# Kernel optimization log

Hardware: AMD Instinct MI355X
Metric: run time of the kernel (lower is better)

Reference implementation:

```python
import jax, jax.numpy as jnp
import numpy as np

NUM_LAYERS = 2
IN_DIM = 256
OUT_DIM = 256
N = 8192


def setup_inputs() -> dict:
    key = jax.random.key(0)
    k = jax.random.split(key, 7)
    x = jax.random.normal(k[0], (N, IN_DIM), dtype=jnp.float32)
    adj = jax.random.uniform(k[1], (N, N), dtype=jnp.float32)
    # MLP params (Linear: y = x @ W.T + b); kaiming-ish scale
    W1 = jax.random.normal(k[2], (OUT_DIM, IN_DIM), dtype=jnp.float32) / np.sqrt(IN_DIM)
    b1 = jnp.zeros((OUT_DIM,), dtype=jnp.float32)
    W2 = jax.random.normal(k[3], (OUT_DIM, OUT_DIM), dtype=jnp.float32) / np.sqrt(OUT_DIM)
    b2 = jnp.zeros((OUT_DIM,), dtype=jnp.float32)
    epsilon = jnp.zeros((1,), dtype=jnp.float32)  # torch init: Tensor([0.0])
    return {"x": x, "adj": adj, "W1": W1, "b1": b1, "W2": W2, "b2": b2, "epsilon": epsilon}


def reference(x, adj, W1, b1, W2, b2, epsilon):
    for _ in range(NUM_LAYERS):
        # epsilon-weighted neighborhood aggregation + residual
        x = x + epsilon * (adj @ x)          # [N, d]
        # 2-layer MLP (shared across layers, as in the torch module)
        h = jax.nn.relu(x @ W1.T + b1)       # [N, out]
        x = h @ W2.T + b2                    # [N, out]
    return x
```

## Files before the change

kernel.cpp:

```cpp
#include <hip/hip_runtime.h>
#include <hip/hip_bf16.h>

typedef __hip_bfloat16 bf16;
typedef short s16x8 __attribute__((ext_vector_type(8)));
typedef float f32x4 __attribute__((ext_vector_type(4)));

static constexpr int NROWS = 8192;
static constexpr int DIM   = 256;

__device__ inline float to_f(float v) { return v; }
__device__ inline float to_f(bf16 v)  { return __bfloat162float(v); }
__device__ inline unsigned short f2bf(float f) {
    bf16 h = __float2bfloat16(f);
    return __builtin_bit_cast(unsigned short, h);
}

__global__ void agg0_convW_kernel(const float* __restrict__ x, const float* __restrict__ adj,
                                  const float* __restrict__ W1, const float* __restrict__ W2,
                                  const float* __restrict__ eps_p,
                                  bf16* __restrict__ W1b, bf16* __restrict__ W2b,
                                  float* __restrict__ y) {
    {
        const int b = blockIdx.x;
        const float* src = (b < 64) ? W1 : W2;
        bf16*       dst = (b < 64) ? W1b : W2b;
        const int t = (b & 63) * 256 + threadIdx.x;
        float4 v = ((const float4*)src)[t];
        ushort4 u = make_ushort4(f2bf(v.x), f2bf(v.y), f2bf(v.z), f2bf(v.w));
        ((ushort4*)dst)[t] = u;
    }
    const float eps = *eps_p;
    if (eps == 0.0f) return;
    const size_t total = (size_t)NROWS * DIM;
    for (size_t e = (size_t)blockIdx.x * blockDim.x + threadIdx.x;
         e < total;
         e += (size_t)gridDim.x * blockDim.x) {
        const int i = (int)(e >> 8);
        const int j = (int)(e & 255);
        float s = 0.0f;
        const float* arow = adj + (size_t)i * NROWS;
        for (int k = 0; k < NROWS; ++k)
            s += arow[k] * x[(size_t)k * DIM + j];
        y[e] = x[e] + eps * s;
    }
}

__global__ void agg1_kernel(const bf16* __restrict__ x, const float* __restrict__ adj,
                            const float* __restrict__ eps_p, bf16* __restrict__ y) {
    const float eps = *eps_p;
    if (eps == 0.0f) return;
    const size_t total = (size_t)NROWS * DIM;
    for (size_t e = (size_t)blockIdx.x * blockDim.x + threadIdx.x;
         e < total;
         e += (size_t)gridDim.x * blockDim.x) {
        const int i = (int)(e >> 8);
        const int j = (int)(e & 255);
        float s = 0.0f;
        const float* arow = adj + (size_t)i * NROWS;
        for (int k = 0; k < NROWS; ++k)
            s += arow[k] * to_f(x[(size_t)k * DIM + j]);
        y[e] = __float2bfloat16(to_f(x[e]) + eps * s);
    }
}

template<typename TIN, bool RELU, bool OUTF32>
__global__ __launch_bounds__(256, 2)
void gemm_bt(const TIN* __restrict__ A0, const TIN* __restrict__ A1,
             const float* __restrict__ eps_p,
             const bf16* __restrict__ W, const float* __restrict__ bias,
             void* __restrict__ C) {
    constexpr int K = 256;
    constexpr int PITCH = 264;
    __shared__ short As[64][PITCH];
    __shared__ short Bs[64][PITCH];

    const TIN* __restrict__ A = (*eps_p == 0.0f) ? A0 : A1;

    const int tid  = threadIdx.x;
    const int lane = tid & 63;
    const int wave = tid >> 6;
    const int wm = (wave & 1) * 32;
    const int wn = (wave >> 1) * 32;
    const int row0 = blockIdx.x * 64;
    const int col0 = blockIdx.y * 64;

#pragma unroll
    for (int p = 0; p < 8; ++p) {
        const int id = p * 256 + tid;
        const int r  = id >> 5;
        const int c  = (id & 31) * 8;
        if constexpr (sizeof(TIN) == 4) {
            const float* src = (const float*)A + (size_t)(row0 + r) * K + c;
            float4 v0 = *(const float4*)(src);
            float4 v1 = *(const float4*)(src + 4);
            ushort4 u0 = make_ushort4(f2bf(v0.x), f2bf(v0.y), f2bf(v0.z), f2bf(v0.w));
            ushort4 u1 = make_ushort4(f2bf(v1.x), f2bf(v1.y), f2bf(v1.z), f2bf(v1.w));
            *(ushort4*)(&As[r][c])     = u0;
            *(ushort4*)(&As[r][c + 4]) = u1;
        } else {
            *(uint4*)(&As[r][c]) = *(const uint4*)((const bf16*)A + (size_t)(row0 + r) * K + c);
        }
        *(uint4*)(&Bs[r][c]) = *(const uint4*)(W + (size_t)(col0 + r) * K + c);
    }
    __syncthreads();

    const int lr = lane & 15;
    const int q  = lane >> 4;
    f32x4 acc[2][2] = {};
#pragma unroll
    for (int kk = 0; kk < 8; ++kk) {
        s16x8 af[2], bf_[2];
#pragma unroll
        for (int i = 0; i < 2; ++i) {
            af[i]  = *(const s16x8*)(&As[wm + i * 16 + lr][kk * 32 + q * 8]);
            bf_[i] = *(const s16x8*)(&Bs[wn + i * 16 + lr][kk * 32 + q * 8]);
        }
#pragma unroll
        for (int i = 0; i < 2; ++i)
#pragma unroll
            for (int j = 0; j < 2; ++j)
                acc[i][j] = __builtin_amdgcn_mfma_f32_16x16x32_bf16(
                    af[i], bf_[j], acc[i][j], 0, 0, 0);
    }

#pragma unroll
    for (int i = 0; i < 2; ++i) {
#pragma unroll
        for (int j = 0; j < 2; ++j) {
            const int col = col0 + wn + j * 16 + lr;
            const float bv = bias[col];
#pragma unroll
            for (int r = 0; r < 4; ++r) {
                const int row = row0 + wm + i * 16 + q * 4 + r;
                float v = acc[i][j][r] + bv;
                if (RELU) v = fmaxf(v, 0.0f);
                if (OUTF32) ((float*)C)[(size_t)row * DIM + col] = v;
                else        ((bf16*)C)[(size_t)row * DIM + col] = __float2bfloat16(v);
            }
        }
    }
}

extern "C" void kernel_launch(void* const* d_in, const int* in_sizes, int n_in,
                              void* d_out, int out_size, void* d_ws, size_t ws_size,
                              hipStream_t stream) {
    const float* x   = (const float*)d_in[0];
    const float* adj = (const float*)d_in[1];
    const float* W1  = (const float*)d_in[2];
    const float* b1  = (const float*)d_in[3];
    const float* W2  = (const float*)d_in[4];
    const float* b2  = (const float*)d_in[5];
    const float* eps = (const float*)d_in[6];
    float* out = (float*)d_out;

    char* ws = (char*)d_ws;
    bf16*  W1b   = (bf16*)ws;  ws += (size_t)DIM * DIM * 2;
    bf16*  W2b   = (bf16*)ws;  ws += (size_t)DIM * DIM * 2;
    bf16*  bufY0 = (bf16*)ws;  ws += (size_t)NROWS * DIM * 2;
    bf16*  bufY1 = (bf16*)ws;  ws += (size_t)NROWS * DIM * 2;
    bf16*  bufY2 = (bf16*)ws;  ws += (size_t)NROWS * DIM * 2;
    float* agg0  = (float*)ws; ws += (size_t)NROWS * DIM * 4;
    bf16*  agg1  = (bf16*)ws;  ws += (size_t)NROWS * DIM * 2;

    const dim3 ggrid(NROWS / 64, DIM / 64);

    agg0_convW_kernel<<<128, 256, 0, stream>>>(x, adj, W1, W2, eps, W1b, W2b, agg0);
    gemm_bt<float, true,  false><<<ggrid, 256, 0, stream>>>(x,     agg0, eps, W1b, b1, bufY0);
    gemm_bt<bf16,  false, false><<<ggrid, 256, 0, stream>>>(bufY0, bufY0, eps, W2b, b2, bufY1);

    agg1_kernel<<<128, 256, 0, stream>>>(bufY1, adj, eps, agg1);
    gemm_bt<bf16,  true,  false><<<ggrid, 256, 0, stream>>>(bufY1, agg1, eps, W1b, b1, bufY2);
    gemm_bt<bf16,  false, true ><<<ggrid, 256, 0, stream>>>(bufY2, bufY2, eps, W2b, b2, out);
}
```

Baseline: 327.6 us.

## Fuse both MLP linears and aggregation into one kernel per layer

Replaces the separate aggregation kernels and four GEMM launches with one fused kernel per layer that optionally aggregates, computes the first linear with ReLU into shared memory, then the second linear. The hidden activation stays in LDS instead of round-tripping through global memory, and launch count drops. Weight fragments are now read directly from global/L2 rather than staged in LDS, and the fallback aggregation path for nonzero epsilon is a naive per-row loop.

Measured after the change: 331.9 us. Within noise of the previous version (+1.3%).

```diff
diff --git a/kernel.cpp b/kernel.cpp
--- a/kernel.cpp
+++ b/kernel.cpp
@@ -15,125 +15,128 @@
     return __builtin_bit_cast(unsigned short, h);
 }
 
-__global__ void agg0_convW_kernel(const float* __restrict__ x, const float* __restrict__ adj,
-                                  const float* __restrict__ W1, const float* __restrict__ W2,
-                                  const float* __restrict__ eps_p,
-                                  bf16* __restrict__ W1b, bf16* __restrict__ W2b,
-                                  float* __restrict__ y) {
-    {
-        const int b = blockIdx.x;
-        const float* src = (b < 64) ? W1 : W2;
-        bf16*       dst = (b < 64) ? W1b : W2b;
-        const int t = (b & 63) * 256 + threadIdx.x;
-        float4 v = ((const float4*)src)[t];
-        ushort4 u = make_ushort4(f2bf(v.x), f2bf(v.y), f2bf(v.z), f2bf(v.w));
-        ((ushort4*)dst)[t] = u;
-    }
-    const float eps = *eps_p;
-    if (eps == 0.0f) return;
-    const size_t total = (size_t)NROWS * DIM;
-    for (size_t e = (size_t)blockIdx.x * blockDim.x + threadIdx.x;
-         e < total;
-         e += (size_t)gridDim.x * blockDim.x) {
-        const int i = (int)(e >> 8);
-        const int j = (int)(e & 255);
-        float s = 0.0f;
-        const float* arow = adj + (size_t)i * NROWS;
-        for (int k = 0; k < NROWS; ++k)
-            s += arow[k] * x[(size_t)k * DIM + j];
-        y[e] = x[e] + eps * s;
-    }
+__global__ void convW_kernel(const float* __restrict__ W1, const float* __restrict__ W2,
+                             bf16* __restrict__ W1b, bf16* __restrict__ W2b) {
+    const int b = blockIdx.x;
+    const float* src = (b < 64) ? W1 : W2;
+    bf16*       dst = (b < 64) ? W1b : W2b;
+    const int t = (b & 63) * 256 + threadIdx.x;
+    float4 v = ((const float4*)src)[t];
+    ((ushort4*)dst)[t] = make_ushort4(f2bf(v.x), f2bf(v.y), f2bf(v.z), f2bf(v.w));
 }
 
-__global__ void agg1_kernel(const bf16* __restrict__ x, const float* __restrict__ adj,
-                            const float* __restrict__ eps_p, bf16* __restrict__ y) {
-    const float eps = *eps_p;
-    if (eps == 0.0f) return;
-    const size_t total = (size_t)NROWS * DIM;
-    for (size_t e = (size_t)blockIdx.x * blockDim.x + threadIdx.x;
-         e < total;
-         e += (size_t)gridDim.x * blockDim.x) {
-        const int i = (int)(e >> 8);
-        const int j = (int)(e & 255);
-        float s = 0.0f;
-        const float* arow = adj + (size_t)i * NROWS;
-        for (int k = 0; k < NROWS; ++k)
-            s += arow[k] * to_f(x[(size_t)k * DIM + j]);
-        y[e] = __float2bfloat16(to_f(x[e]) + eps * s);
-    }
-}
-
-template<typename TIN, bool RELU, bool OUTF32>
-__global__ __launch_bounds__(256, 2)
-void gemm_bt(const TIN* __restrict__ A0, const TIN* __restrict__ A1,
-             const float* __restrict__ eps_p,
-             const bf16* __restrict__ W, const float* __restrict__ bias,
-             void* __restrict__ C) {
+template<typename TIN, bool OUTF32>
+__global__ __launch_bounds__(256, 1)
+void fused_mlp(const TIN* __restrict__ A, const float* __restrict__ adj,
+               const float* __restrict__ eps_p,
+               const bf16* __restrict__ W1, const float* __restrict__ b1,
+               const bf16* __restrict__ W2, const float* __restrict__ b2,
+               void* __restrict__ C) {
     constexpr int K = 256;
     constexpr int PITCH = 264;
-    __shared__ short As[64][PITCH];
-    __shared__ short Bs[64][PITCH];
-
-    const TIN* __restrict__ A = (*eps_p == 0.0f) ? A0 : A1;
+    __shared__ short Xs[32][PITCH];
+    __shared__ short Hs[32][PITCH];
 
     const int tid  = threadIdx.x;
     const int lane = tid & 63;
     const int wave = tid >> 6;
-    const int wm = (wave & 1) * 32;
-    const int wn = (wave >> 1) * 32;
-    const int row0 = blockIdx.x * 64;
-    const int col0 = blockIdx.y * 64;
+    const int lr = lane & 15;
+    const int q  = lane >> 4;
+    const int row0 = blockIdx.x * 32;
+    const float eps = *eps_p;
 
+    if (eps == 0.0f) {
 #pragma unroll
-    for (int p = 0; p < 8; ++p) {
-        const int id = p * 256 + tid;
-        const int r  = id >> 5;
-        const int c  = (id & 31) * 8;
-        if constexpr (sizeof(TIN) == 4) {
-            const float* src = (const float*)A + (size_t)(row0 + r) * K + c;
-            float4 v0 = *(const float4*)(src);
-            float4 v1 = *(const float4*)(src + 4);
-            ushort4 u0 = make_ushort4(f2bf(v0.x), f2bf(v0.y), f2bf(v0.z), f2bf(v0.w));
-            ushort4 u1 = make_ushort4(f2bf(v1.x), f2bf(v1.y), f2bf(v1.z), f2bf(v1.w));
-            *(ushort4*)(&As[r][c])     = u0;
-            *(ushort4*)(&As[r][c + 4]) = u1;
-        } else {
-            *(uint4*)(&As[r][c]) = *(const uint4*)((const bf16*)A + (size_t)(row0 + r) * K + c);
+        for (int p = 0; p < 4; ++p) {
+            const int id = p * 256 + tid;
+            const int r  = id >> 5;
+            const int c  = (id & 31) * 8;
+            if constexpr (sizeof(TIN) == 4) {
+                const float* src = (const float*)A + (size_t)(row0 + r) * K + c;
+                float4 v0 = *(const float4*)(src);
+                float4 v1 = *(const float4*)(src + 4);
+                *(ushort4*)(&Xs[r][c])     = make_ushort4(f2bf(v0.x), f2bf(v0.y), f2bf(v0.z), f2bf(v0.w));
+                *(ushort4*)(&Xs[r][c + 4]) = make_ushort4(f2bf(v1.x), f2bf(v1.y), f2bf(v1.z), f2bf(v1.w));
+            } else {
+                *(uint4*)(&Xs[r][c]) = *(const uint4*)((const bf16*)A + (size_t)(row0 + r) * K + c);
+            }
         }
-        *(uint4*)(&Bs[r][c]) = *(const uint4*)(W + (size_t)(col0 + r) * K + c);
+    } else {
+        for (int r = 0; r < 32; ++r) {
+            const int row = row0 + r;
+            float s = 0.0f;
+            const float* arow = adj + (size_t)row * NROWS;
+            for (int k = 0; k < NROWS; ++k)
+                s += arow[k] * to_f(A[(size_t)k * DIM + tid]);
+            Xs[r][tid] = (short)f2bf(to_f(A[(size_t)row * DIM + tid]) + eps * s);
+        }
     }
     __syncthreads();
 
-    const int lr = lane & 15;
-    const int q  = lane >> 4;
-    f32x4 acc[2][2] = {};
+    f32x4 acc1[4][2] = {};
+    const bf16* W1p = W1 + (size_t)(wave * 64 + lr) * K + q * 8;
 #pragma unroll
     for (int kk = 0; kk < 8; ++kk) {
-        s16x8 af[2], bf_[2];
+        s16x8 wf[4], xf[2];
 #pragma unroll
-        for (int i = 0; i < 2; ++i) {
-            af[i]  = *(const s16x8*)(&As[wm + i * 16 + lr][kk * 32 + q * 8]);
-            bf_[i] = *(const s16x8*)(&Bs[wn + i * 16 + lr][kk * 32 + q * 8]);
+        for (int i = 0; i < 4; ++i)
+            wf[i] = *(const s16x8*)(W1p + (size_t)i * 16 * K + kk * 32);
+#pragma unroll
+        for (int j = 0; j < 2; ++j)
+            xf[j] = *(const s16x8*)(&Xs[j * 16 + lr][kk * 32 + q * 8]);
+#pragma unroll
+        for (int i = 0; i < 4; ++i)
+#pragma unroll
+            for (int j = 0; j < 2; ++j)
+                acc1[i][j] = __builtin_amdgcn_mfma_f32_16x16x32_bf16(
+                    wf[i], xf[j], acc1[i][j], 0, 0, 0);
+    }
+
+#pragma unroll
+    for (int i = 0; i < 4; ++i) {
+        const int hc = wave * 64 + i * 16 + q * 4;
+        const float4 bv = *(const float4*)(b1 + hc);
+#pragma unroll
+        for (int j = 0; j < 2; ++j) {
+            ushort4 hv;
+            hv.x = f2bf(fmaxf(acc1[i][j][0] + bv.x, 0.0f));
+            hv.y = f2bf(fmaxf(acc1[i][j][1] + bv.y, 0.0f));
+            hv.z = f2bf(fmaxf(acc1[i][j][2] + bv.z, 0.0f));
+            hv.w = f2bf(fmaxf(acc1[i][j][3] + bv.w, 0.0f));
+            *(ushort4*)(&Hs[j * 16 + lr][hc]) = hv;
         }
+    }
+    __syncthreads();
+
+    f32x4 acc2[2][4] = {};
+    const bf16* W2p = W2 + (size_t)(wave * 64 + lr) * K + q * 8;
+#pragma unroll
+    for (int kk = 0; kk < 8; ++kk) {
+        s16x8 hf[2], wf[4];
+#pragma unroll
+        for (int j = 0; j < 4; ++j)
+            wf[j] = *(const s16x8*)(W2p + (size_t)j * 16 * K + kk * 32);
+#pragma unroll
+        for (int i = 0; i < 2; ++i)
+            hf[i] = *(const s16x8*)(&Hs[i * 16 + lr][kk * 32 + q * 8]);
 #pragma unroll
         for (int i = 0; i < 2; ++i)
 #pragma unroll
-            for (int j = 0; j < 2; ++j)
-                acc[i][j] = __builtin_amdgcn_mfma_f32_16x16x32_bf16(
-                    af[i], bf_[j], acc[i][j], 0, 0, 0);
+            for (int j = 0; j < 4; ++j)
+                acc2[i][j] = __builtin_amdgcn_mfma_f32_16x16x32_bf16(
+                    hf[i], wf[j], acc2[i][j], 0, 0, 0);
     }
 
 #pragma unroll
     for (int i = 0; i < 2; ++i) {
 #pragma unroll
-        for (int j = 0; j < 2; ++j) {
-            const int col = col0 + wn + j * 16 + lr;
-            const float bv = bias[col];
+        for (int j = 0; j < 4; ++j) {
+            const int col = wave * 64 + j * 16 + lr;
+            const float bv = b2[col];
 #pragma unroll
             for (int r = 0; r < 4; ++r) {
-                const int row = row0 + wm + i * 16 + q * 4 + r;
-                float v = acc[i][j][r] + bv;
-                if (RELU) v = fmaxf(v, 0.0f);
+                const int row = row0 + i * 16 + q * 4 + r;
+                float v = acc2[i][j][r] + bv;
                 if (OUTF32) ((float*)C)[(size_t)row * DIM + col] = v;
                 else        ((bf16*)C)[(size_t)row * DIM + col] = __float2bfloat16(v);
             }
@@ -154,21 +157,11 @@
     float* out = (float*)d_out;
 
     char* ws = (char*)d_ws;
-    bf16*  W1b   = (bf16*)ws;  ws += (size_t)DIM * DIM * 2;
-    bf16*  W2b   = (bf16*)ws;  ws += (size_t)DIM * DIM * 2;
-    bf16*  bufY0 = (bf16*)ws;  ws += (size_t)NROWS * DIM * 2;
-    bf16*  bufY1 = (bf16*)ws;  ws += (size_t)NROWS * DIM * 2;
-    bf16*  bufY2 = (bf16*)ws;  ws += (size_t)NROWS * DIM * 2;
-    float* agg0  = (float*)ws; ws += (size_t)NROWS * DIM * 4;
-    bf16*  agg1  = (bf16*)ws;  ws += (size_t)NROWS * DIM * 2;
+    bf16* W1b   = (bf16*)ws;  ws += (size_t)DIM * DIM * 2;
+    bf16* W2b   = (bf16*)ws;  ws += (size_t)DIM * DIM * 2;
+    bf16* bufY1 = (bf16*)ws;  ws += (size_t)NROWS * DIM * 2;
 
-    const dim3 ggrid(NROWS / 64, DIM / 64);
-
-    agg0_convW_kernel<<<128, 256, 0, stream>>>(x, adj, W1, W2, eps, W1b, W2b, agg0);
-    gemm_bt<float, true,  false><<<ggrid, 256, 0, stream>>>(x,     agg0, eps, W1b, b1, bufY0);
-    gemm_bt<bf16,  false, false><<<ggrid, 256, 0, stream>>>(bufY0, bufY0, eps, W2b, b2, bufY1);
-
-    agg1_kernel<<<128, 256, 0, stream>>>(bufY1, adj, eps, agg1);
-    gemm_bt<bf16,  true,  false><<<ggrid, 256, 0, stream>>>(bufY1, agg1, eps, W1b, b1, bufY2);
-    gemm_bt<bf16,  false, true ><<<ggrid, 256, 0, stream>>>(bufY2, bufY2, eps, W2b, b2, out);
+    convW_kernel<<<128, 256, 0, stream>>>(W1, W2, W1b, W2b);
+    fused_mlp<float, false><<<NROWS / 32, 256, 0, stream>>>(x, adj, eps, W1b, b1, W2b, b2, bufY1);
+    fused_mlp<bf16,  true ><<<NROWS / 32, 256, 0, stream>>>(bufY1, adj, eps, W1b, b1, W2b, b2, out);
 }
```
